# Kernel optimization log

Hardware: AMD Instinct MI355X
Metric: run time of the kernel (lower is better)

Reference implementation:

```python
import jax, jax.numpy as jnp
import numpy as np

EMB = 512
HEADS = 8
B, T = 4, 1024


def setup_inputs() -> dict:
    key = jax.random.key(0)
    k1, k2, k3, k4, k5 = jax.random.split(key, 5)
    scale = 1.0 / np.sqrt(EMB)
    x = jax.random.normal(k1, (B, T, EMB), dtype=jnp.float32)
    # Linear(emb, emb*heads, bias=False) weights, stored as [in, out] for x @ W
    Wk = jax.random.normal(k2, (EMB, EMB * HEADS), dtype=jnp.float32) * scale
    Wq = jax.random.normal(k3, (EMB, EMB * HEADS), dtype=jnp.float32) * scale
    Wv = jax.random.normal(k4, (EMB, EMB * HEADS), dtype=jnp.float32) * scale
    Wu = jax.random.normal(k5, (EMB * HEADS, EMB), dtype=jnp.float32) * (1.0 / np.sqrt(EMB * HEADS))
    return {"x": x, "Wk": Wk, "Wq": Wq, "Wv": Wv, "Wu": Wu}


def reference(x, Wk, Wq, Wv, Wu):
    b, t, k = x.shape
    h = HEADS
    # projections -> [b, h, t, k]
    keys = (x @ Wk).reshape(b, t, h, k).transpose(0, 2, 1, 3)
    queries = (x @ Wq).reshape(b, t, h, k).transpose(0, 2, 1, 3)
    values = (x @ Wv).reshape(b, t, h, k).transpose(0, 2, 1, 3)
    # NOTE: original computes bmm(keys, queries^T): dot[i,j] = key_i . query_j
    dot = jnp.einsum('bhik,bhjk->bhij', keys, queries)  # [b,h,t,t]
    # mask_fn: only upper-triangle (offset=1) entries that are EXACTLY zero get -inf
    triu = jnp.triu(jnp.ones((t, t), dtype=bool), k=1)
    final_mask = triu & (dot == 0)
    dot = jnp.where(final_mask, -jnp.inf, dot)
    attn = jax.nn.softmax(dot, axis=-1)
    out = jnp.einsum('bhij,bhjk->bhik', attn, values)  # [b,h,t,k]
    out = out.transpose(0, 2, 1, 3).reshape(b, t, h * k)
    return out @ Wu
```

## Files before the change

kernel.cpp:

```cpp
#include <hip/hip_runtime.h>
#include <stdint.h>

typedef _Float16 f16x8 __attribute__((ext_vector_type(8)));
typedef float f32x4 __attribute__((ext_vector_type(4)));

__device__ __forceinline__ unsigned short f2h(float f) {
  _Float16 h = (_Float16)f;
  return __builtin_bit_cast(unsigned short, h);
}

#if __has_builtin(__builtin_amdgcn_global_load_lds)
#define HAVE_GLL 1
__device__ __forceinline__ void gload_lds16(const void* g, void* l) {
  auto gp = reinterpret_cast<const __attribute__((address_space(1))) void*>(
      reinterpret_cast<uintptr_t>(g));
  auto lp = reinterpret_cast<__attribute__((address_space(3))) void*>(
      reinterpret_cast<uintptr_t>(l));
  __builtin_amdgcn_global_load_lds(gp, lp, 16, 0, 0);
}
#else
#define HAVE_GLL 0
#endif

template <int OUT, int BVU>
__device__ __forceinline__ void gemm_core(unsigned short* __restrict__ As,
                                          unsigned short* __restrict__ Bs,
                                          const unsigned short* __restrict__ A,
                                          const unsigned short* __restrict__ B,
                                          void* __restrict__ Cv, int K, int lda, int ldb,
                                          int ldc, long coff, int m0, int n0, int kbase) {
  int tid = threadIdx.x;
  int wid = tid >> 6, lane = tid & 63;
  int wm = (wid >> 1) * 64, wn = (wid & 1) * 64;
  int rq = lane >> 4, rl = lane & 15;

  f32x4 acc[4][4];
#pragma unroll
  for (int i = 0; i < 4; ++i)
#pragma unroll
    for (int j = 0; j < 4; ++j) acc[i][j] = (f32x4){0.f, 0.f, 0.f, 0.f};

#if HAVE_GLL
  int cg = (lane & 7) ^ ((lane >> 3) & 7);
  int rl8 = lane >> 3;
#endif

  for (int k0 = 0; k0 < K; k0 += 64) {
    long bko;
    if (BVU) {
      int kk = kbase + k0;
      bko = (long)(kk >> 10) * 2097152 + (kk & 1023);
    } else {
      bko = k0;
    }
    __syncthreads();
#if HAVE_GLL
#pragma unroll
    for (int t = 0; t < 4; ++t) {
      int r = wid * 32 + t * 8;
      gload_lds16(&A[(long)(m0 + r + rl8) * lda + k0 + cg * 8], &As[r * 64]);
      gload_lds16(&B[(long)(n0 + r + rl8) * ldb + bko + cg * 8], &Bs[r * 64]);
    }
#else
#pragma unroll
    for (int it = 0; it < 4; ++it) {
      int idx = tid + it * 256;
      int r = idx >> 3, c = idx & 7;
      int cs = c ^ (r & 7);
      *reinterpret_cast<uint4*>(&As[r * 64 + cs * 8]) =
          *reinterpret_cast<const uint4*>(&A[(long)(m0 + r) * lda + k0 + c * 8]);
      *reinterpret_cast<uint4*>(&Bs[r * 64 + cs * 8]) =
          *reinterpret_cast<const uint4*>(&B[(long)(n0 + r) * ldb + bko + c * 8]);
    }
#endif
    __syncthreads();
#pragma unroll
    for (int ks = 0; ks < 2; ++ks) {
      f16x8 af[4], bfr[4];
      int kc = ks * 4 + rq;
#pragma unroll
      for (int i = 0; i < 4; ++i) {
        int ra = wm + i * 16 + rl;
        af[i] = *reinterpret_cast<const f16x8*>(&As[ra * 64 + ((kc ^ (ra & 7)) << 3)]);
        int rb = wn + i * 16 + rl;
        bfr[i] = *reinterpret_cast<const f16x8*>(&Bs[rb * 64 + ((kc ^ (rb & 7)) << 3)]);
      }
#pragma unroll
      for (int i = 0; i < 4; ++i)
#pragma unroll
        for (int j = 0; j < 4; ++j)
          acc[i][j] = __builtin_amdgcn_mfma_f32_16x16x32_f16(af[i], bfr[j], acc[i][j], 0, 0, 0);
    }
  }

#pragma unroll
  for (int i = 0; i < 4; ++i)
#pragma unroll
    for (int j = 0; j < 4; ++j)
#pragma unroll
      for (int r = 0; r < 4; ++r) {
        int row = m0 + wm + i * 16 + rq * 4 + r;
        int col = n0 + wn + j * 16 + rl;
        float v = acc[i][j][r];
        if (OUT == 1)
          reinterpret_cast<unsigned short*>(Cv)[coff + (long)row * ldc + col] = f2h(v);
        else
          reinterpret_cast<float*>(Cv)[coff + (long)row * ldc + col] = v;
      }
}

__device__ __forceinline__ void w_core(unsigned short* __restrict__ As,
                                       unsigned short* __restrict__ Bs,
                                       const float* __restrict__ A32,
                                       const float* __restrict__ B32,
                                       unsigned short* __restrict__ C,
                                       int lda, int ldb, bool atrans, int m0, int n0) {
  int tid = threadIdx.x;
  int wid = tid >> 6, lane = tid & 63;
  int wm = (wid >> 1) * 64, wn = (wid & 1) * 64;
  int rq = lane >> 4, rl = lane & 15;

  f32x4 acc[4][4];
#pragma unroll
  for (int i = 0; i < 4; ++i)
#pragma unroll
    for (int j = 0; j < 4; ++j) acc[i][j] = (f32x4){0.f, 0.f, 0.f, 0.f};

  for (int k0 = 0; k0 < 512; k0 += 64) {
    __syncthreads();
    if (!atrans) {
#pragma unroll
      for (int it = 0; it < 8; ++it) {
        int idx = it * 256 + tid;
        int r = idx >> 4, kq = idx & 15;
        float4 v = *reinterpret_cast<const float4*>(&A32[(long)(m0 + r) * lda + k0 + kq * 4]);
        ushort4 u;
        u.x = f2h(v.x); u.y = f2h(v.y); u.z = f2h(v.z); u.w = f2h(v.w);
        int cs = (kq >> 1) ^ (r & 7);
        *reinterpret_cast<ushort4*>(&As[r * 64 + cs * 8 + (kq & 1) * 4]) = u;
      }
    } else {
#pragma unroll
      for (int it = 0; it < 32; ++it) {
        int idx = it * 256 + tid;
        int m = idx & 127, d = idx >> 7;
        float v = A32[(long)(k0 + d) * 512 + m0 + m];
        int cs = (d >> 3) ^ (m & 7);
        As[m * 64 + cs * 8 + (d & 7)] = f2h(v);
      }
    }
#pragma unroll
    for (int it = 0; it < 8; ++it) {
      int idx = it * 256 + tid;
      int r = idx >> 4, kq = idx & 15;
      float4 v = *reinterpret_cast<const float4*>(&B32[(long)(n0 + r) * ldb + k0 + kq * 4]);
      ushort4 u;
      u.x = f2h(v.x); u.y = f2h(v.y); u.z = f2h(v.z); u.w = f2h(v.w);
      int cs = (kq >> 1) ^ (r & 7);
      *reinterpret_cast<ushort4*>(&Bs[r * 64 + cs * 8 + (kq & 1) * 4]) = u;
    }
    __syncthreads();
#pragma unroll
    for (int ks = 0; ks < 2; ++ks) {
      f16x8 af[4], bfr[4];
      int kc = ks * 4 + rq;
#pragma unroll
      for (int i = 0; i < 4; ++i) {
        int ra = wm + i * 16 + rl;
        af[i] = *reinterpret_cast<const f16x8*>(&As[ra * 64 + ((kc ^ (ra & 7)) << 3)]);
        int rb = wn + i * 16 + rl;
        bfr[i] = *reinterpret_cast<const f16x8*>(&Bs[rb * 64 + ((kc ^ (rb & 7)) << 3)]);
      }
#pragma unroll
      for (int i = 0; i < 4; ++i)
#pragma unroll
        for (int j = 0; j < 4; ++j)
          acc[i][j] = __builtin_amdgcn_mfma_f32_16x16x32_f16(af[i], bfr[j], acc[i][j], 0, 0, 0);
    }
  }

#pragma unroll
  for (int i = 0; i < 4; ++i)
#pragma unroll
    for (int j = 0; j < 4; ++j)
#pragma unroll
      for (int r = 0; r < 4; ++r) {
        int row = m0 + wm + i * 16 + rq * 4 + r;
        int col = n0 + wn + j * 16 + rl;
        C[(long)row * 512 + col] = f2h(acc[i][j][r]);
      }
}

#define DECL_LDS \
  __shared__ unsigned short As[128 * 64]; \
  __shared__ unsigned short Bs[128 * 64];

__global__ __launch_bounds__(256, 2) void k_wsetup(
    const float* __restrict__ x, const float* __restrict__ Wq, const float* __restrict__ Wk,
    const float* __restrict__ Wv, const float* __restrict__ Wu,
    unsigned short* __restrict__ Xh, unsigned short* __restrict__ Gt,
    unsigned short* __restrict__ Wvut) {
  DECL_LDS
  int c = blockIdx.x, w = blockIdx.y;
  if (w >= 32) {
    int i = ((w - 32) * 8 + c) * 256 + threadIdx.x;
    float4 v = reinterpret_cast<const float4*>(x)[i];
    ushort4 u;
    u.x = f2h(v.x); u.y = f2h(v.y); u.z = f2h(v.z); u.w = f2h(v.w);
    reinterpret_cast<ushort4*>(Xh)[i] = u;
    return;
  }
  const float *A32, *B32;
  unsigned short* C;
  int lda;
  bool atrans;
  int t;
  if (w < 16) {
    A32 = Wq + c * 512; B32 = Wk + c * 512; C = Gt + (long)c * 262144;
    lda = 4096; atrans = false; t = w;
  } else {
    A32 = Wu + (long)c * 262144; B32 = Wv + c * 512; C = Wvut + (long)c * 262144;
    lda = 512; atrans = true; t = w - 16;
  }
  w_core(As, Bs, A32, B32, C, lda, 4096, atrans, (t >> 2) * 128, (t & 3) * 128);
}

__global__ __launch_bounds__(256, 2) void k_gemm_tv(
    const unsigned short* __restrict__ X, const unsigned short* __restrict__ Gt,
    const unsigned short* __restrict__ Wvut, unsigned short* __restrict__ T,
    unsigned short* __restrict__ VUt) {
  DECL_LDS
  int c = blockIdx.x, w = blockIdx.y;
  const unsigned short *A, *B;
  unsigned short* C;
  long coff;
  int m0, n0;
  if (w < 128) {
    A = X; B = Gt + (long)c * 262144; C = T;
    coff = (long)c * 512; m0 = (w >> 2) * 128; n0 = (w & 3) * 128;
  } else {
    int wp = w - 128;
    A = Wvut; B = X; C = VUt;
    coff = 0; m0 = (4 * c + (wp & 3)) * 128; n0 = (wp >> 2) * 128;
  }
  gemm_core<1, 0>(As, Bs, A, B, C, 512, 512, 512, 4096, coff, m0, n0, 0);
}

__global__ __launch_bounds__(256, 2) void k_gemm_s(
    const unsigned short* __restrict__ X, const unsigned short* __restrict__ T,
    unsigned short* __restrict__ Pb) {
  DECL_LDS
  int c = blockIdx.x, w = blockIdx.y;
  int z = c + 8 * (w >> 6), t = w & 63;
  int b = z >> 3, h = z & 7;
  gemm_core<1, 0>(As, Bs, T + (long)b * 4194304 + h * 512, X + (long)b * 524288, Pb,
                  512, 4096, 512, 8192, (long)b * 8388608 + h * 1024,
                  (t >> 3) * 128, (t & 7) * 128, 0);
}

__global__ __launch_bounds__(256, 2) void k_gemm_out(
    const unsigned short* __restrict__ Pb, const unsigned short* __restrict__ VUt,
    float* __restrict__ Opart) {
  DECL_LDS
  int c = blockIdx.x, w = blockIdx.y;
  int g = c + 8 * (w >> 4);
  int r = w & 15;
  int b = g >> 3, kc = (g >> 1) & 3, ih = g & 1;
  int y = ih * 4 + (r >> 2);
  int x = r & 3;
  gemm_core<0, 1>(As, Bs, Pb + (long)b * 8388608 + kc * 2048, VUt + (long)b * 1024,
                  Opart, 2048, 8192, 4096, 512,
                  (long)kc * 2097152 + (long)b * 524288, y * 128, x * 128, kc * 2048);
}

__global__ __launch_bounds__(256) void k_reduce(const float* __restrict__ Opart,
                                                float* __restrict__ out) {
  int i = blockIdx.x * 256 + threadIdx.x;
  float4 a = reinterpret_cast<const float4*>(Opart)[i];
  float4 b = reinterpret_cast<const float4*>(Opart + 2097152)[i];
  float4 c = reinterpret_cast<const float4*>(Opart + 4194304)[i];
  float4 d = reinterpret_cast<const float4*>(Opart + 6291456)[i];
  float4 o;
  o.x = (a.x + b.x) + (c.x + d.x);
  o.y = (a.y + b.y) + (c.y + d.y);
  o.z = (a.z + b.z) + (c.z + d.z);
  o.w = (a.w + b.w) + (c.w + d.w);
  reinterpret_cast<float4*>(out)[i] = o;
}

__global__ __launch_bounds__(256) void k_softmax_x(unsigned short* __restrict__ S) {
  int g = blockIdx.y * 4 + (threadIdx.x >> 6);
  int b = g >> 10, i = g & 1023;
  long base = (long)b * 8388608 + (long)i * 8192 + (long)blockIdx.x * 1024;
  int lane = threadIdx.x & 63;
  f16x8* p = reinterpret_cast<f16x8*>(S + base);
  f16x8 a = p[lane * 2], bb = p[lane * 2 + 1];
  float v[16];
#pragma unroll
  for (int q = 0; q < 8; ++q) { v[q] = (float)a[q]; v[8 + q] = (float)bb[q]; }
  float m = v[0];
#pragma unroll
  for (int q = 1; q < 16; ++q) m = fmaxf(m, v[q]);
#pragma unroll
  for (int o = 32; o; o >>= 1) m = fmaxf(m, __shfl_xor(m, o));
  float s = 0.f;
#pragma unroll
  for (int q = 0; q < 16; ++q) { v[q] = __expf(v[q] - m); s += v[q]; }
#pragma unroll
  for (int o = 32; o; o >>= 1) s += __shfl_xor(s, o);
  float inv = 1.0f / s;
  f16x8 oa, ob;
#pragma unroll
  for (int q = 0; q < 8; ++q) {
    oa[q] = (_Float16)(v[q] * inv);
    ob[q] = (_Float16)(v[8 + q] * inv);
  }
  p[lane * 2] = oa;
  p[lane * 2 + 1] = ob;
}

__global__ void k_sentinel(float* out, float v) { out[0] = v; }

extern "C" void kernel_launch(void* const* d_in, const int* in_sizes, int n_in,
                              void* d_out, int out_size, void* d_ws, size_t ws_size,
                              hipStream_t stream) {
  const float* x  = (const float*)d_in[0];
  const float* Wk = (const float*)d_in[1];
  const float* Wq = (const float*)d_in[2];
  const float* Wv = (const float*)d_in[3];
  const float* Wu = (const float*)d_in[4];
  float* out = (float*)d_out;

  const long SZ_X = 4096L * 512;
  const size_t NEED = 150994944;

  if (ws_size < NEED) {
    hipMemsetAsync(d_out, 0, (size_t)out_size * 4, stream);
    k_sentinel<<<1, 1, 0, stream>>>(out, (float)ws_size);
    return;
  }

  char* p = (char*)d_ws;
  unsigned short* Xbf  = (unsigned short*)p; p += SZ_X * 2;
  unsigned short* Wvut = (unsigned short*)p; p += 8L * 512 * 512 * 2;
  unsigned short* Gt   = (unsigned short*)p; p += 8L * 512 * 512 * 2;
  unsigned short* T    = (unsigned short*)p; p += 4096L * 4096 * 2;
  unsigned short* Pb   = (unsigned short*)p; p += 4096L * 8192 * 2;
  unsigned short* VUt  = (unsigned short*)p;
  float* Opart = (float*)T;

  k_wsetup<<<dim3(8, 288), 256, 0, stream>>>(x, Wq, Wk, Wv, Wu, Xbf, Gt, Wvut);

  k_gemm_tv<<<dim3(8, 256), 256, 0, stream>>>(Xbf, Gt, Wvut, T, VUt);

  k_gemm_s<<<dim3(8, 256), 256, 0, stream>>>(Xbf, T, Pb);

  k_softmax_x<<<dim3(8, 1024), 256, 0, stream>>>(Pb);

  k_gemm_out<<<dim3(8, 64), 256, 0, stream>>>(Pb, VUt, Opart);

  k_reduce<<<2048, 256, 0, stream>>>(Opart, out);
}
```

Baseline: 242.5 us.

## Use 256x256-tile 8-wave GEMM core for projection and score GEMMs

Adds a new GEMM core that computes 256x256 output tiles with 512 threads. It double-buffers LDS with direct global-to-LDS loads, XOR-swizzled reads and split-phase barriers that interleave MFMA with the next stage's loads. The tv and score kernels now launch 4x fewer, larger blocks, aiming for more data reuse per LDS load and better overlap. The cost is higher register and LDS use per block (128 KB of LDS), fewer blocks overall and a risk of lower occupancy or tail imbalance.

```diff
diff --git a/kernel.cpp b/kernel.cpp
--- a/kernel.cpp
+++ b/kernel.cpp
@@ -21,6 +21,174 @@
 #else
 #define HAVE_GLL 0
 #endif
+
+#if HAVE_GLL
+#define WAITV(n) asm volatile("s_waitcnt vmcnt(" #n ")" ::: "memory")
+#else
+#define WAITV(n) asm volatile("s_waitcnt lgkmcnt(0)" ::: "memory")
+#endif
+#define WAITL0                                        \
+  asm volatile("s_waitcnt lgkmcnt(0)" ::: "memory"); \
+  __builtin_amdgcn_sched_barrier(0)
+#define BAR __builtin_amdgcn_s_barrier()
+
+template <int NT>
+__device__ __forceinline__ void gemm_core256(unsigned short* __restrict__ Ls,
+                                             const unsigned short* __restrict__ A,
+                                             const unsigned short* __restrict__ B,
+                                             unsigned short* __restrict__ C, int lda,
+                                             int ldb, int ldc, long coff, int m0, int n0) {
+  unsigned short* As = Ls;
+  unsigned short* Bs = Ls + 32768;
+  const int tid = threadIdx.x;
+  const int wid = tid >> 6, lane = tid & 63;
+  const int wm = (wid >> 2) * 128, wn = (wid & 3) * 64;
+  const int rq = lane >> 4, rl = lane & 15;
+  const int phi = (rl >> 1) & 3;
+
+  f32x4 acc[8][4];
+#pragma unroll
+  for (int i = 0; i < 8; ++i)
+#pragma unroll
+    for (int j = 0; j < 4; ++j) acc[i][j] = (f32x4){0.f, 0.f, 0.f, 0.f};
+
+  const int cg = (((lane & 3) ^ ((lane >> 3) & 3)) << 3);
+  const int rr = lane >> 2;
+  const unsigned short* Ag = &A[(long)(m0 + wid * 32 + rr) * lda + cg];
+  const unsigned short* Bg = &B[(long)(n0 + wid * 32 + rr) * ldb + cg];
+  unsigned short* AsW = As + wid * 1024;
+  unsigned short* BsW = Bs + wid * 1024;
+  const long a16 = (long)16 * lda, b16 = (long)16 * ldb;
+
+  auto stageA = [&](int buf, int kh, int kcol) {
+    unsigned short* d = AsW + (buf * 2 + kh) * 8192;
+    const unsigned short* g = Ag + kcol + (kh << 5);
+#if HAVE_GLL
+    gload_lds16(g, d);
+    gload_lds16(g + a16, d + 512);
+#else
+    *reinterpret_cast<uint4*>(d + lane * 8) = *reinterpret_cast<const uint4*>(g);
+    *reinterpret_cast<uint4*>(d + 512 + lane * 8) =
+        *reinterpret_cast<const uint4*>(g + a16);
+#endif
+  };
+  auto stageB = [&](int buf, int kh, int kcol) {
+    unsigned short* d = BsW + (buf * 2 + kh) * 8192;
+    const unsigned short* g = Bg + kcol + (kh << 5);
+#if HAVE_GLL
+    gload_lds16(g, d);
+    gload_lds16(g + b16, d + 512);
+#else
+    *reinterpret_cast<uint4*>(d + lane * 8) = *reinterpret_cast<const uint4*>(g);
+    *reinterpret_cast<uint4*>(d + 512 + lane * 8) =
+        *reinterpret_cast<const uint4*>(g + b16);
+#endif
+  };
+  auto rdA = [&](f16x8* af, int buf, int ks, int qi) {
+    const unsigned short* p = As + (buf * 2 + ks) * 8192;
+#pragma unroll
+    for (int i = 0; i < 4; ++i) {
+      int ra = wm + qi * 64 + i * 16 + rl;
+      af[i] = *reinterpret_cast<const f16x8*>(&p[ra * 32 + ((rq ^ phi) << 3)]);
+    }
+  };
+  auto rdB = [&](f16x8* bf, int buf, int ks) {
+    const unsigned short* p = Bs + (buf * 2 + ks) * 8192;
+#pragma unroll
+    for (int j = 0; j < 4; ++j) {
+      int rb = wn + j * 16 + rl;
+      bf[j] = *reinterpret_cast<const f16x8*>(&p[rb * 32 + ((rq ^ phi) << 3)]);
+    }
+  };
+  auto mm = [&](f16x8* af, f16x8* bf, int qi) {
+    __builtin_amdgcn_s_setprio(1);
+#pragma unroll
+    for (int i = 0; i < 4; ++i)
+#pragma unroll
+      for (int j = 0; j < 4; ++j)
+        acc[qi * 4 + i][j] = __builtin_amdgcn_mfma_f32_16x16x32_f16(
+            af[i], bf[j], acc[qi * 4 + i][j], 0, 0, 0);
+    __builtin_amdgcn_s_setprio(0);
+  };
+
+  stageA(0, 0, 0);
+  stageB(0, 0, 0);
+  stageA(0, 1, 0);
+  stageB(0, 1, 0);
+  WAITV(4);
+  BAR;
+
+  for (int t = 0; t < NT - 1; ++t) {
+    const int cur = t & 1, nxt = cur ^ 1;
+    const int kn = (t + 1) * 64;
+    f16x8 a0[4], a1[4], b0[4], b1[4];
+    rdA(a0, cur, 0, 0);
+    rdB(b0, cur, 0);
+    stageA(nxt, 0, kn);
+    BAR;
+    WAITL0;
+    mm(a0, b0, 0);
+    BAR;
+    rdA(a1, cur, 0, 1);
+    stageB(nxt, 0, kn);
+    BAR;
+    WAITL0;
+    mm(a1, b0, 1);
+    WAITV(4);
+    BAR;
+    rdA(a0, cur, 1, 0);
+    rdB(b1, cur, 1);
+    stageA(nxt, 1, kn);
+    BAR;
+    WAITL0;
+    mm(a0, b1, 0);
+    BAR;
+    rdA(a1, cur, 1, 1);
+    stageB(nxt, 1, kn);
+    BAR;
+    WAITL0;
+    mm(a1, b1, 1);
+    WAITV(4);
+    BAR;
+  }
+  {
+    const int cur = (NT - 1) & 1;
+    f16x8 a0[4], a1[4], b0[4], b1[4];
+    rdA(a0, cur, 0, 0);
+    rdB(b0, cur, 0);
+    BAR;
+    WAITL0;
+    mm(a0, b0, 0);
+    BAR;
+    rdA(a1, cur, 0, 1);
+    BAR;
+    WAITL0;
+    mm(a1, b0, 1);
+    WAITV(0);
+    BAR;
+    rdA(a0, cur, 1, 0);
+    rdB(b1, cur, 1);
+    BAR;
+    WAITL0;
+    mm(a0, b1, 0);
+    BAR;
+    rdA(a1, cur, 1, 1);
+    BAR;
+    WAITL0;
+    mm(a1, b1, 1);
+  }
+
+#pragma unroll
+  for (int i = 0; i < 8; ++i)
+#pragma unroll
+    for (int j = 0; j < 4; ++j)
+#pragma unroll
+      for (int r = 0; r < 4; ++r) {
+        int row = m0 + wm + i * 16 + rq * 4 + r;
+        int col = n0 + wn + j * 16 + rl;
+        C[coff + (long)row * ldc + col] = f2h(acc[i][j][r]);
+      }
+}
 
 template <int OUT, int BVU>
 __device__ __forceinline__ void gemm_core(unsigned short* __restrict__ As,
@@ -225,37 +393,36 @@
   w_core(As, Bs, A32, B32, C, lda, 4096, atrans, (t >> 2) * 128, (t & 3) * 128);
 }
 
-__global__ __launch_bounds__(256, 2) void k_gemm_tv(
+__global__ __launch_bounds__(512, 2) void k_gemm_tv(
     const unsigned short* __restrict__ X, const unsigned short* __restrict__ Gt,
     const unsigned short* __restrict__ Wvut, unsigned short* __restrict__ T,
     unsigned short* __restrict__ VUt) {
-  DECL_LDS
+  __shared__ unsigned short Ls[65536];
   int c = blockIdx.x, w = blockIdx.y;
   const unsigned short *A, *B;
   unsigned short* C;
   long coff;
   int m0, n0;
-  if (w < 128) {
+  if (w < 32) {
     A = X; B = Gt + (long)c * 262144; C = T;
-    coff = (long)c * 512; m0 = (w >> 2) * 128; n0 = (w & 3) * 128;
+    coff = (long)c * 512; m0 = (w >> 1) * 256; n0 = (w & 1) * 256;
   } else {
-    int wp = w - 128;
+    int wp = w - 32;
     A = Wvut; B = X; C = VUt;
-    coff = 0; m0 = (4 * c + (wp & 3)) * 128; n0 = (wp >> 2) * 128;
-  }
-  gemm_core<1, 0>(As, Bs, A, B, C, 512, 512, 512, 4096, coff, m0, n0, 0);
-}
-
-__global__ __launch_bounds__(256, 2) void k_gemm_s(
+    coff = 0; m0 = c * 512 + (wp & 1) * 256; n0 = (wp >> 1) * 256;
+  }
+  gemm_core256<8>(Ls, A, B, C, 512, 512, 4096, coff, m0, n0);
+}
+
+__global__ __launch_bounds__(512, 2) void k_gemm_s(
     const unsigned short* __restrict__ X, const unsigned short* __restrict__ T,
     unsigned short* __restrict__ Pb) {
-  DECL_LDS
+  __shared__ unsigned short Ls[65536];
   int c = blockIdx.x, w = blockIdx.y;
-  int z = c + 8 * (w >> 6), t = w & 63;
-  int b = z >> 3, h = z & 7;
-  gemm_core<1, 0>(As, Bs, T + (long)b * 4194304 + h * 512, X + (long)b * 524288, Pb,
-                  512, 4096, 512, 8192, (long)b * 8388608 + h * 1024,
-                  (t >> 3) * 128, (t & 7) * 128, 0);
+  int b = w >> 4, t = w & 15;
+  gemm_core256<8>(Ls, T + (long)b * 4194304 + c * 512, X + (long)b * 524288, Pb,
+                  4096, 512, 8192, (long)b * 8388608 + c * 1024,
+                  ((t >> 2) & 3) * 256, (t & 3) * 256);
 }
 
 __global__ __launch_bounds__(256, 2) void k_gemm_out(
@@ -351,9 +518,9 @@
 
   k_wsetup<<<dim3(8, 288), 256, 0, stream>>>(x, Wq, Wk, Wv, Wu, Xbf, Gt, Wvut);
 
-  k_gemm_tv<<<dim3(8, 256), 256, 0, stream>>>(Xbf, Gt, Wvut, T, VUt);
-
-  k_gemm_s<<<dim3(8, 256), 256, 0, stream>>>(Xbf, T, Pb);
+  k_gemm_tv<<<dim3(8, 64), 512, 0, stream>>>(Xbf, Gt, Wvut, T, VUt);
+
+  k_gemm_s<<<dim3(8, 64), 512, 0, stream>>>(Xbf, T, Pb);
 
   k_softmax_x<<<dim3(8, 1024), 256, 0, stream>>>(Pb);
 
```

Result: slower. 262.1 us (+8.1%).

## Fuse softmax into score GEMM epilogue with per-tile stats and rescale in output GEMM

Applied to the files above, without the earlier changes.

The score GEMM now exponentiates each 128x128 tile against its local row max in the epilogue, writes the unnormalized f16 values, and stores per-tile (max, sum) stats. The output GEMM combines those stats into per-row correction factors and rescales the A tile while loading it through registers. This drops the separate softmax kernel and its full read and write pass over the score matrix. In exchange, the output GEMM's A operand no longer uses direct global-to-LDS loads, adding conversion work there, and the score GEMM epilogue gains extra LDS reductions and syncs.

```diff
diff --git a/kernel.cpp b/kernel.cpp
--- a/kernel.cpp
+++ b/kernel.cpp
@@ -22,13 +22,14 @@
 #define HAVE_GLL 0
 #endif
 
-template <int OUT, int BVU>
+template <int OUT, int BVU, int SMAX>
 __device__ __forceinline__ void gemm_core(unsigned short* __restrict__ As,
                                           unsigned short* __restrict__ Bs,
                                           const unsigned short* __restrict__ A,
                                           const unsigned short* __restrict__ B,
                                           void* __restrict__ Cv, int K, int lda, int ldb,
-                                          int ldc, long coff, int m0, int n0, int kbase) {
+                                          int ldc, long coff, int m0, int n0, int kbase,
+                                          float2* __restrict__ stats, long sbase) {
   int tid = threadIdx.x;
   int wid = tid >> 6, lane = tid & 63;
   int wm = (wid >> 1) * 64, wn = (wid & 1) * 64;
@@ -90,6 +91,48 @@
 #pragma unroll
         for (int j = 0; j < 4; ++j)
           acc[i][j] = __builtin_amdgcn_mfma_f32_16x16x32_f16(af[i], bfr[j], acc[i][j], 0, 0, 0);
+    }
+  }
+
+  if constexpr (SMAX) {
+    __syncthreads();
+    float* tmx = reinterpret_cast<float*>(As);
+    float* tsm = tmx + 256;
+    int wp = wid & 1;
+#pragma unroll
+    for (int i = 0; i < 4; ++i)
+#pragma unroll
+      for (int r = 0; r < 4; ++r) {
+        float mx = fmaxf(fmaxf(acc[i][0][r], acc[i][1][r]),
+                         fmaxf(acc[i][2][r], acc[i][3][r]));
+#pragma unroll
+        for (int o = 1; o < 16; o <<= 1) mx = fmaxf(mx, __shfl_xor(mx, o));
+        if (rl == 0) tmx[wp * 128 + wm + i * 16 + rq * 4 + r] = mx;
+      }
+    __syncthreads();
+#pragma unroll
+    for (int i = 0; i < 4; ++i)
+#pragma unroll
+      for (int r = 0; r < 4; ++r) {
+        int row = wm + i * 16 + rq * 4 + r;
+        float m = fmaxf(tmx[row], tmx[128 + row]);
+        float s = 0.f;
+#pragma unroll
+        for (int j = 0; j < 4; ++j) {
+          float e = __expf(acc[i][j][r] - m);
+          acc[i][j][r] = e;
+          s += e;
+        }
+#pragma unroll
+        for (int o = 1; o < 16; o <<= 1) s += __shfl_xor(s, o);
+        if (rl == 0) tsm[wp * 128 + row] = s;
+      }
+    __syncthreads();
+    if (tid < 128) {
+      int row = tid;
+      float m = fmaxf(tmx[row], tmx[128 + row]);
+      float s = tsm[row] + tsm[128 + row];
+      stats[sbase + (long)row * 8] = make_float2(m, s);
     }
   }
 
@@ -243,34 +286,146 @@
     A = Wvut; B = X; C = VUt;
     coff = 0; m0 = (4 * c + (wp & 3)) * 128; n0 = (wp >> 2) * 128;
   }
-  gemm_core<1, 0>(As, Bs, A, B, C, 512, 512, 512, 4096, coff, m0, n0, 0);
+  gemm_core<1, 0, 0>(As, Bs, A, B, C, 512, 512, 512, 4096, coff, m0, n0, 0, nullptr, 0);
 }
 
 __global__ __launch_bounds__(256, 2) void k_gemm_s(
     const unsigned short* __restrict__ X, const unsigned short* __restrict__ T,
-    unsigned short* __restrict__ Pb) {
+    unsigned short* __restrict__ Pb, float2* __restrict__ stats) {
   DECL_LDS
   int c = blockIdx.x, w = blockIdx.y;
   int z = c + 8 * (w >> 6), t = w & 63;
   int b = z >> 3, h = z & 7;
-  gemm_core<1, 0>(As, Bs, T + (long)b * 4194304 + h * 512, X + (long)b * 524288, Pb,
-                  512, 4096, 512, 8192, (long)b * 8388608 + h * 1024,
-                  (t >> 3) * 128, (t & 7) * 128, 0);
+  long sbase = (((long)b * 8 + h) * 1024 + (t >> 3) * 128) * 8 + (t & 7);
+  gemm_core<1, 0, 1>(As, Bs, T + (long)b * 4194304 + h * 512, X + (long)b * 524288, Pb,
+                     512, 4096, 512, 8192, (long)b * 8388608 + h * 1024,
+                     (t >> 3) * 128, (t & 7) * 128, 0, stats, sbase);
 }
 
 __global__ __launch_bounds__(256, 2) void k_gemm_out(
     const unsigned short* __restrict__ Pb, const unsigned short* __restrict__ VUt,
-    float* __restrict__ Opart) {
-  DECL_LDS
+    const float2* __restrict__ stats, float* __restrict__ Opart) {
+  __shared__ unsigned short As[128 * 64];
+  __shared__ unsigned short Bs[128 * 64];
+  __shared__ float fct[128 * 16];
+  __shared__ float MH[256];
+  __shared__ float IH[256];
   int c = blockIdx.x, w = blockIdx.y;
   int g = c + 8 * (w >> 4);
   int r = w & 15;
   int b = g >> 3, kc = (g >> 1) & 3, ih = g & 1;
   int y = ih * 4 + (r >> 2);
   int x = r & 3;
-  gemm_core<0, 1>(As, Bs, Pb + (long)b * 8388608 + kc * 2048, VUt + (long)b * 1024,
-                  Opart, 2048, 8192, 4096, 512,
-                  (long)kc * 2097152 + (long)b * 524288, y * 128, x * 128, kc * 2048);
+  int m0 = y * 128, n0 = x * 128;
+  const unsigned short* A = Pb + (long)b * 8388608 + kc * 2048;
+  const unsigned short* Bp = VUt + (long)b * 1024;
+
+  {
+    int t = threadIdx.x, row = t >> 1, hh = t & 1;
+    long sb = (((long)b * 8 + kc * 2 + hh) * 1024 + m0 + row) * 8;
+    float2 st[8];
+    float m = -3.4e38f;
+#pragma unroll
+    for (int k = 0; k < 8; ++k) { st[k] = stats[sb + k]; m = fmaxf(m, st[k].x); }
+    float s = 0.f;
+#pragma unroll
+    for (int k = 0; k < 8; ++k) s += st[k].y * __expf(st[k].x - m);
+    MH[t] = m;
+    IH[t] = 1.0f / s;
+  }
+  __syncthreads();
+#pragma unroll
+  for (int it = 0; it < 8; ++it) {
+    int idx = threadIdx.x + it * 256;
+    int row = idx >> 4, sg = idx & 15;
+    int hh = sg >> 3, seg = sg & 7;
+    float mseg = stats[(((long)b * 8 + kc * 2 + hh) * 1024 + m0 + row) * 8 + seg].x;
+    fct[row * 16 + sg] = __expf(mseg - MH[row * 2 + hh]) * IH[row * 2 + hh];
+  }
+
+  int tid = threadIdx.x;
+  int wid = tid >> 6, lane = tid & 63;
+  int wm = (wid >> 1) * 64, wn = (wid & 1) * 64;
+  int rq = lane >> 4, rl = lane & 15;
+  f32x4 acc[4][4];
+#pragma unroll
+  for (int i = 0; i < 4; ++i)
+#pragma unroll
+    for (int j = 0; j < 4; ++j) acc[i][j] = (f32x4){0.f, 0.f, 0.f, 0.f};
+#if HAVE_GLL
+  int cg = (lane & 7) ^ ((lane >> 3) & 7);
+  int rl8 = lane >> 3;
+#endif
+
+  for (int k0 = 0; k0 < 2048; k0 += 64) {
+    int kk = kc * 2048 + k0;
+    long bko = (long)(kk >> 10) * 2097152 + (kk & 1023);
+    __syncthreads();
+#pragma unroll
+    for (int it = 0; it < 4; ++it) {
+      int idx = tid + it * 256;
+      int rr = idx >> 3, cc = idx & 7;
+      uint4 raw = *reinterpret_cast<const uint4*>(&A[(long)(m0 + rr) * 8192 + k0 + cc * 8]);
+      float f = fct[rr * 16 + (k0 >> 7)];
+      uint vv[4] = {raw.x, raw.y, raw.z, raw.w};
+#pragma unroll
+      for (int q = 0; q < 4; ++q) {
+        _Float16 lo = __builtin_bit_cast(_Float16, (unsigned short)(vv[q] & 0xffffu));
+        _Float16 hi = __builtin_bit_cast(_Float16, (unsigned short)(vv[q] >> 16));
+        unsigned short slo = f2h((float)lo * f);
+        unsigned short shi = f2h((float)hi * f);
+        vv[q] = (uint)slo | ((uint)shi << 16);
+      }
+      uint4 outv = {vv[0], vv[1], vv[2], vv[3]};
+      *reinterpret_cast<uint4*>(&As[rr * 64 + ((cc ^ (rr & 7)) << 3)]) = outv;
+    }
+#if HAVE_GLL
+#pragma unroll
+    for (int t2 = 0; t2 < 4; ++t2) {
+      int rr2 = wid * 32 + t2 * 8;
+      gload_lds16(&Bp[(long)(n0 + rr2 + rl8) * 4096 + bko + cg * 8], &Bs[rr2 * 64]);
+    }
+#else
+#pragma unroll
+    for (int it = 0; it < 4; ++it) {
+      int idx = tid + it * 256;
+      int rr2 = idx >> 3, cc = idx & 7;
+      int cs = cc ^ (rr2 & 7);
+      *reinterpret_cast<uint4*>(&Bs[rr2 * 64 + cs * 8]) =
+          *reinterpret_cast<const uint4*>(&Bp[(long)(n0 + rr2) * 4096 + bko + cc * 8]);
+    }
+#endif
+    __syncthreads();
+#pragma unroll
+    for (int ks = 0; ks < 2; ++ks) {
+      f16x8 af[4], bfr[4];
+      int kcx = ks * 4 + rq;
+#pragma unroll
+      for (int i = 0; i < 4; ++i) {
+        int ra = wm + i * 16 + rl;
+        af[i] = *reinterpret_cast<const f16x8*>(&As[ra * 64 + ((kcx ^ (ra & 7)) << 3)]);
+        int rb = wn + i * 16 + rl;
+        bfr[i] = *reinterpret_cast<const f16x8*>(&Bs[rb * 64 + ((kcx ^ (rb & 7)) << 3)]);
+      }
+#pragma unroll
+      for (int i = 0; i < 4; ++i)
+#pragma unroll
+        for (int j = 0; j < 4; ++j)
+          acc[i][j] = __builtin_amdgcn_mfma_f32_16x16x32_f16(af[i], bfr[j], acc[i][j], 0, 0, 0);
+    }
+  }
+
+  long coff = (long)kc * 2097152 + (long)b * 524288;
+#pragma unroll
+  for (int i = 0; i < 4; ++i)
+#pragma unroll
+    for (int j = 0; j < 4; ++j)
+#pragma unroll
+      for (int rr = 0; rr < 4; ++rr) {
+        int row = m0 + wm + i * 16 + rq * 4 + rr;
+        int col = n0 + wn + j * 16 + rl;
+        Opart[coff + (long)row * 512 + col] = acc[i][j][rr];
+      }
 }
 
 __global__ __launch_bounds__(256) void k_reduce(const float* __restrict__ Opart,
@@ -288,37 +443,6 @@
   reinterpret_cast<float4*>(out)[i] = o;
 }
 
-__global__ __launch_bounds__(256) void k_softmax_x(unsigned short* __restrict__ S) {
-  int g = blockIdx.y * 4 + (threadIdx.x >> 6);
-  int b = g >> 10, i = g & 1023;
-  long base = (long)b * 8388608 + (long)i * 8192 + (long)blockIdx.x * 1024;
-  int lane = threadIdx.x & 63;
-  f16x8* p = reinterpret_cast<f16x8*>(S + base);
-  f16x8 a = p[lane * 2], bb = p[lane * 2 + 1];
-  float v[16];
-#pragma unroll
-  for (int q = 0; q < 8; ++q) { v[q] = (float)a[q]; v[8 + q] = (float)bb[q]; }
-  float m = v[0];
-#pragma unroll
-  for (int q = 1; q < 16; ++q) m = fmaxf(m, v[q]);
-#pragma unroll
-  for (int o = 32; o; o >>= 1) m = fmaxf(m, __shfl_xor(m, o));
-  float s = 0.f;
-#pragma unroll
-  for (int q = 0; q < 16; ++q) { v[q] = __expf(v[q] - m); s += v[q]; }
-#pragma unroll
-  for (int o = 32; o; o >>= 1) s += __shfl_xor(s, o);
-  float inv = 1.0f / s;
-  f16x8 oa, ob;
-#pragma unroll
-  for (int q = 0; q < 8; ++q) {
-    oa[q] = (_Float16)(v[q] * inv);
-    ob[q] = (_Float16)(v[8 + q] * inv);
-  }
-  p[lane * 2] = oa;
-  p[lane * 2 + 1] = ob;
-}
-
 __global__ void k_sentinel(float* out, float v) { out[0] = v; }
 
 extern "C" void kernel_launch(void* const* d_in, const int* in_sizes, int n_in,
@@ -346,18 +470,17 @@
   unsigned short* Gt   = (unsigned short*)p; p += 8L * 512 * 512 * 2;
   unsigned short* T    = (unsigned short*)p; p += 4096L * 4096 * 2;
   unsigned short* Pb   = (unsigned short*)p; p += 4096L * 8192 * 2;
-  unsigned short* VUt  = (unsigned short*)p;
+  unsigned short* VUt  = (unsigned short*)p; p += 4096L * 4096 * 2;
+  float2* Stats = (float2*)p;
   float* Opart = (float*)T;
 
   k_wsetup<<<dim3(8, 288), 256, 0, stream>>>(x, Wq, Wk, Wv, Wu, Xbf, Gt, Wvut);
 
   k_gemm_tv<<<dim3(8, 256), 256, 0, stream>>>(Xbf, Gt, Wvut, T, VUt);
 
-  k_gemm_s<<<dim3(8, 256), 256, 0, stream>>>(Xbf, T, Pb);
-
-  k_softmax_x<<<dim3(8, 1024), 256, 0, stream>>>(Pb);
-
-  k_gemm_out<<<dim3(8, 64), 256, 0, stream>>>(Pb, VUt, Opart);
+  k_gemm_s<<<dim3(8, 256), 256, 0, stream>>>(Xbf, T, Pb, Stats);
+
+  k_gemm_out<<<dim3(8, 64), 256, 0, stream>>>(Pb, VUt, Stats, Opart);
 
   k_reduce<<<2048, 256, 0, stream>>>(Opart, out);
 }
```

Measured after the change: 251.9 us. +3.9%, slower.

## Fuse split-K reduction into output GEMM and vectorize transposed weight loads

Applied to the files above, without the earlier changes.

Removes the separate k_reduce kernel. Each k_gemm_out block bumps an atomic counter for its output tile, and the last of the four split-K blocks sums the four fp32 partials and writes the final output. A hipMemsetAsync is added to clear the counters before each run. Separately, the transposed-weight load in the setup kernel now reads float4 vectors instead of scalar strided loads. The fusion saves a launch and the reduce pass, at the cost of an extra memset, threadfences and atomics, plus a serialized tail in the last-arriving blocks.

```diff
diff --git a/kernel.cpp b/kernel.cpp
--- a/kernel.cpp
+++ b/kernel.cpp
@@ -41,7 +41,7 @@
     for (int j = 0; j < 4; ++j) acc[i][j] = (f32x4){0.f, 0.f, 0.f, 0.f};
 
 #if HAVE_GLL
-  int cg = (lane & 7) ^ ((lane >> 3) & 7);
+  int cg_ = (lane & 7) ^ ((lane >> 3) & 7);
   int rl8 = lane >> 3;
 #endif
 
@@ -58,8 +58,8 @@
 #pragma unroll
     for (int t = 0; t < 4; ++t) {
       int r = wid * 32 + t * 8;
-      gload_lds16(&A[(long)(m0 + r + rl8) * lda + k0 + cg * 8], &As[r * 64]);
-      gload_lds16(&B[(long)(n0 + r + rl8) * ldb + bko + cg * 8], &Bs[r * 64]);
+      gload_lds16(&A[(long)(m0 + r + rl8) * lda + k0 + cg_ * 8], &As[r * 64]);
+      gload_lds16(&B[(long)(n0 + r + rl8) * ldb + bko + cg_ * 8], &Bs[r * 64]);
     }
 #else
 #pragma unroll
@@ -141,12 +141,17 @@
       }
     } else {
 #pragma unroll
-      for (int it = 0; it < 32; ++it) {
+      for (int it = 0; it < 8; ++it) {
         int idx = it * 256 + tid;
-        int m = idx & 127, d = idx >> 7;
-        float v = A32[(long)(k0 + d) * 512 + m0 + m];
-        int cs = (d >> 3) ^ (m & 7);
-        As[m * 64 + cs * 8 + (d & 7)] = f2h(v);
+        int d = idx >> 5, mq = (idx & 31) << 2;
+        float4 v = *reinterpret_cast<const float4*>(&A32[(long)(k0 + d) * 512 + m0 + mq]);
+        float vv[4] = {v.x, v.y, v.z, v.w};
+#pragma unroll
+        for (int q = 0; q < 4; ++q) {
+          int m = mq + q;
+          int cs = (d >> 3) ^ (m & 7);
+          As[m * 64 + cs * 8 + (d & 7)] = f2h(vv[q]);
+        }
       }
     }
 #pragma unroll
@@ -258,9 +263,40 @@
                   (t >> 3) * 128, (t & 7) * 128, 0);
 }
 
+__global__ __launch_bounds__(256) void k_softmax_x(unsigned short* __restrict__ S) {
+  int g = blockIdx.y * 4 + (threadIdx.x >> 6);
+  int b = g >> 10, i = g & 1023;
+  long base = (long)b * 8388608 + (long)i * 8192 + (long)blockIdx.x * 1024;
+  int lane = threadIdx.x & 63;
+  f16x8* p = reinterpret_cast<f16x8*>(S + base);
+  f16x8 a = p[lane * 2], bb = p[lane * 2 + 1];
+  float v[16];
+#pragma unroll
+  for (int q = 0; q < 8; ++q) { v[q] = (float)a[q]; v[8 + q] = (float)bb[q]; }
+  float m = v[0];
+#pragma unroll
+  for (int q = 1; q < 16; ++q) m = fmaxf(m, v[q]);
+#pragma unroll
+  for (int o = 32; o; o >>= 1) m = fmaxf(m, __shfl_xor(m, o));
+  float s = 0.f;
+#pragma unroll
+  for (int q = 0; q < 16; ++q) { v[q] = __expf(v[q] - m); s += v[q]; }
+#pragma unroll
+  for (int o = 32; o; o >>= 1) s += __shfl_xor(s, o);
+  float inv = 1.0f / s;
+  f16x8 oa, ob;
+#pragma unroll
+  for (int q = 0; q < 8; ++q) {
+    oa[q] = (_Float16)(v[q] * inv);
+    ob[q] = (_Float16)(v[8 + q] * inv);
+  }
+  p[lane * 2] = oa;
+  p[lane * 2 + 1] = ob;
+}
+
 __global__ __launch_bounds__(256, 2) void k_gemm_out(
     const unsigned short* __restrict__ Pb, const unsigned short* __restrict__ VUt,
-    float* __restrict__ Opart) {
+    float* __restrict__ Opart, float* __restrict__ out, int* __restrict__ cnt) {
   DECL_LDS
   int c = blockIdx.x, w = blockIdx.y;
   int g = c + 8 * (w >> 4);
@@ -271,52 +307,34 @@
   gemm_core<0, 1>(As, Bs, Pb + (long)b * 8388608 + kc * 2048, VUt + (long)b * 1024,
                   Opart, 2048, 8192, 4096, 512,
                   (long)kc * 2097152 + (long)b * 524288, y * 128, x * 128, kc * 2048);
-}
-
-__global__ __launch_bounds__(256) void k_reduce(const float* __restrict__ Opart,
-                                                float* __restrict__ out) {
-  int i = blockIdx.x * 256 + threadIdx.x;
-  float4 a = reinterpret_cast<const float4*>(Opart)[i];
-  float4 b = reinterpret_cast<const float4*>(Opart + 2097152)[i];
-  float4 c = reinterpret_cast<const float4*>(Opart + 4194304)[i];
-  float4 d = reinterpret_cast<const float4*>(Opart + 6291456)[i];
-  float4 o;
-  o.x = (a.x + b.x) + (c.x + d.x);
-  o.y = (a.y + b.y) + (c.y + d.y);
-  o.z = (a.z + b.z) + (c.z + d.z);
-  o.w = (a.w + b.w) + (c.w + d.w);
-  reinterpret_cast<float4*>(out)[i] = o;
-}
-
-__global__ __launch_bounds__(256) void k_softmax_x(unsigned short* __restrict__ S) {
-  int g = blockIdx.y * 4 + (threadIdx.x >> 6);
-  int b = g >> 10, i = g & 1023;
-  long base = (long)b * 8388608 + (long)i * 8192 + (long)blockIdx.x * 1024;
-  int lane = threadIdx.x & 63;
-  f16x8* p = reinterpret_cast<f16x8*>(S + base);
-  f16x8 a = p[lane * 2], bb = p[lane * 2 + 1];
-  float v[16];
-#pragma unroll
-  for (int q = 0; q < 8; ++q) { v[q] = (float)a[q]; v[8 + q] = (float)bb[q]; }
-  float m = v[0];
-#pragma unroll
-  for (int q = 1; q < 16; ++q) m = fmaxf(m, v[q]);
-#pragma unroll
-  for (int o = 32; o; o >>= 1) m = fmaxf(m, __shfl_xor(m, o));
-  float s = 0.f;
-#pragma unroll
-  for (int q = 0; q < 16; ++q) { v[q] = __expf(v[q] - m); s += v[q]; }
-#pragma unroll
-  for (int o = 32; o; o >>= 1) s += __shfl_xor(s, o);
-  float inv = 1.0f / s;
-  f16x8 oa, ob;
-#pragma unroll
-  for (int q = 0; q < 8; ++q) {
-    oa[q] = (_Float16)(v[q] * inv);
-    ob[q] = (_Float16)(v[8 + q] * inv);
-  }
-  p[lane * 2] = oa;
-  p[lane * 2 + 1] = ob;
+
+  __threadfence();
+  __shared__ int lastflag;
+  if (threadIdx.x == 0) {
+    int region = (b * 8 + y) * 4 + x;
+    lastflag = (atomicAdd(&cnt[region], 1) == 3);
+  }
+  __syncthreads();
+  if (!lastflag) return;
+  __threadfence();
+
+  long base0 = (long)b * 524288 + (long)(y * 128) * 512 + x * 128;
+#pragma unroll
+  for (int t = 0; t < 16; ++t) {
+    int lin = threadIdx.x + t * 256;
+    int rr = lin >> 5, c4 = (lin & 31) * 4;
+    long o = base0 + (long)rr * 512 + c4;
+    float4 a = *reinterpret_cast<const float4*>(Opart + o);
+    float4 bq = *reinterpret_cast<const float4*>(Opart + 2097152 + o);
+    float4 cq = *reinterpret_cast<const float4*>(Opart + 4194304 + o);
+    float4 dq = *reinterpret_cast<const float4*>(Opart + 6291456 + o);
+    float4 ov;
+    ov.x = (a.x + bq.x) + (cq.x + dq.x);
+    ov.y = (a.y + bq.y) + (cq.y + dq.y);
+    ov.z = (a.z + bq.z) + (cq.z + dq.z);
+    ov.w = (a.w + bq.w) + (cq.w + dq.w);
+    *reinterpret_cast<float4*>(out + o) = ov;
+  }
 }
 
 __global__ void k_sentinel(float* out, float v) { out[0] = v; }
@@ -346,9 +364,12 @@
   unsigned short* Gt   = (unsigned short*)p; p += 8L * 512 * 512 * 2;
   unsigned short* T    = (unsigned short*)p; p += 4096L * 4096 * 2;
   unsigned short* Pb   = (unsigned short*)p; p += 4096L * 8192 * 2;
-  unsigned short* VUt  = (unsigned short*)p;
+  unsigned short* VUt  = (unsigned short*)p; p += 4096L * 4096 * 2;
+  int* Cnt = (int*)p;
   float* Opart = (float*)T;
 
+  hipMemsetAsync(Cnt, 0, 128 * sizeof(int), stream);
+
   k_wsetup<<<dim3(8, 288), 256, 0, stream>>>(x, Wq, Wk, Wv, Wu, Xbf, Gt, Wvut);
 
   k_gemm_tv<<<dim3(8, 256), 256, 0, stream>>>(Xbf, Gt, Wvut, T, VUt);
@@ -357,7 +378,5 @@
 
   k_softmax_x<<<dim3(8, 1024), 256, 0, stream>>>(Pb);
 
-  k_gemm_out<<<dim3(8, 64), 256, 0, stream>>>(Pb, VUt, Opart);
-
-  k_reduce<<<2048, 256, 0, stream>>>(Opart, out);
-}
+  k_gemm_out<<<dim3(8, 64), 256, 0, stream>>>(Pb, VUt, Opart, out, Cnt);
+}
```

New measurement: 355.6 us. +46.7%, slower.
